# Optimization experiments

Measured on AMD Instinct MI355X. Metric: run time of the kernel, lower is better.

Reference implementation:

```python
import jax, jax.numpy as jnp
import numpy as np

K = 20
EPS = 1e-5
NEG_SLOPE = 0.2


def setup_inputs() -> dict:
    key = jax.random.key(0)
    k1, k2, k3, k4 = jax.random.split(key, 4)
    B, C, N, O = 8, 64, 4096, 64
    x = jax.random.normal(k1, (B, C, N), dtype=jnp.float32)
    # Conv2d(2C, O, kernel_size=1, bias=False) -> weight [O, 2C]
    W = jax.random.normal(k2, (O, 2 * C), dtype=jnp.float32) * (1.0 / np.sqrt(2 * C))
    gamma = jnp.ones((O,), dtype=jnp.float32)
    beta = jnp.zeros((O,), dtype=jnp.float32)
    return {"x": x, "W": W, "gamma": gamma, "beta": beta}


def reference(x, W, gamma, beta):
    B, C, N = x.shape
    xt = jnp.transpose(x, (0, 2, 1))  # [B, N, C]
    # knn: negative squared pairwise distance, topk -> nearest neighbors
    inner = jnp.einsum('bic,bjc->bij', xt, xt)  # [B, N, N]
    xx = jnp.sum(xt * xt, axis=-1)              # [B, N]
    neg_dist = 2.0 * inner - xx[:, :, None] - xx[:, None, :]
    _, idx = jax.lax.top_k(neg_dist, K)         # [B, N, K]
    # gather neighbor features: [B, N, K, C]
    feature = jax.vmap(lambda f, i: f[i])(xt, idx)
    x_central = jnp.broadcast_to(xt[:, :, None, :], (B, N, K, C))
    edge = jnp.concatenate([feature - x_central, x_central], axis=-1)  # [B, N, K, 2C]
    # 1x1 conv == matmul over channel dim
    y = jnp.einsum('bnkc,oc->bnko', edge, W)    # [B, N, K, O]
    # BatchNorm2d in training mode: batch stats over (B, N, K) per channel
    mean = jnp.mean(y, axis=(0, 1, 2))
    var = jnp.var(y, axis=(0, 1, 2))
    y = (y - mean) * jax.lax.rsqrt(var + EPS) * gamma + beta
    y = jnp.where(y >= 0, y, NEG_SLOPE * y)     # LeakyReLU(0.2)
    out = jnp.max(y, axis=2)                    # max over k neighbors -> [B, N, O]
    return jnp.transpose(out, (0, 2, 1))        # [B, O, N]
```

## Files before the change

kernel.cpp:

```cpp
#include <hip/hip_runtime.h>
#include <cstdint>
#include <cstddef>

#define BB 8
#define CC 64
#define NN 4096
#define OO 64
#define KK 20
#define TWO_C 128
#define BN (BB * NN)

#define GSPLIT 16
#define GJPB (NN / GSPLIT)
#define CSPLIT 4
#define CJPB (NN / CSPLIT)
#define SEGCAP 32

typedef float vf4 __attribute__((ext_vector_type(4)));
typedef float f4  __attribute__((ext_vector_type(4)));
typedef _Float16 hf2 __attribute__((ext_vector_type(2)));
typedef _Float16 h8  __attribute__((ext_vector_type(8)));

__device__ __forceinline__ unsigned int pack_h2(float a, float b) {
    hf2 h; h.x = (_Float16)a; h.y = (_Float16)b;
    return __builtin_bit_cast(unsigned int, h);
}

__device__ __forceinline__ unsigned int fmap(float d) {
    unsigned int s = __float_as_uint(d);
    return s ^ (unsigned int)(((int)s >> 31) | 0x80000000);
}

__device__ __forceinline__ unsigned long long cmpx(unsigned long long key, int lane, int j, bool dirDesc) {
    unsigned long long o = __shfl_xor(key, j, 64);
    bool lower = (lane & j) == 0;
    bool takeMax = (dirDesc == lower);
    return ((o > key) == takeMax) ? o : key;
}

__global__ __launch_bounds__(256) void transpose_kernel(const float* __restrict__ x,
                                                        float* __restrict__ xT,
                                                        unsigned int* __restrict__ xTh) {
    __shared__ float t[64][65];
    const int b = blockIdx.y;
    const int n0 = blockIdx.x * 64;
    const int tid = threadIdx.x;
    const int ln = tid & 63, g = tid >> 6;
#pragma unroll
    for (int i = 0; i < 16; ++i) {
        int c = g * 16 + i;
        t[c][ln] = x[((size_t)b * CC + c) * NN + n0 + ln];
    }
    __syncthreads();
#pragma unroll
    for (int i = 0; i < 16; ++i) {
        int nl = g * 16 + i;
        xT[((size_t)b * NN + n0 + nl) * CC + ln] = t[ln][nl];
    }
#pragma unroll
    for (int it = 0; it < 8; ++it) {
        int e = it * 256 + tid;
        int nl = e >> 5, cp = e & 31;
        xTh[((size_t)b * NN + n0 + nl) * 32 + cp] = pack_h2(t[2*cp][nl], t[2*cp+1][nl]);
    }
}

__global__ __launch_bounds__(256) void xx_kernel(const float* __restrict__ x,
                                                 float* __restrict__ xx) {
    int t = blockIdx.x * 256 + threadIdx.x;
    int b = t >> 12, n = t & (NN - 1);
    const float* xp = x + (size_t)b * CC * NN + n;
    float acc = 0.f;
#pragma unroll
    for (int c = 0; c < CC; ++c) {
        float v = xp[(size_t)c * NN];
        acc += v * v;
    }
    xx[t] = acc;
}

__global__ __launch_bounds__(256) void knn_gmax_kernel(const unsigned int* __restrict__ xTh,
                                                       const float* __restrict__ xx,
                                                       float* __restrict__ gmaxG) {
    const int tid = threadIdx.x;
    const int wv = tid >> 6, lane = tid & 63;
    const int lcol = lane & 15, lrow = lane >> 4;
    const int b = blockIdx.z;
    const int i0w = blockIdx.x * 256 + wv * 64;
    const int j0 = blockIdx.y * GJPB;
    const unsigned int* xb = xTh + (size_t)b * NN * 32;
    const float* xxb = xx + (size_t)b * NN;

    uint4 A0[4], A1[4];
#pragma unroll
    for (int s = 0; s < 4; ++s) {
        const uint4* ap = (const uint4*)(xb + (size_t)(i0w + s * 16 + lcol) * 32 + lrow * 4);
        A0[s] = ap[0]; A1[s] = ap[4];
    }

    int g = j0 >> 7;
    for (int gg = 0; gg < GJPB / 128; ++gg, ++g) {
        float m[16];
#pragma unroll
        for (int s = 0; s < 16; ++s) m[s] = -3.4e38f;
#pragma unroll
        for (int jt = 0; jt < 8; ++jt) {
            const int jj = j0 + gg * 128 + jt * 16 + lcol;
            const uint4* bp = (const uint4*)(xb + (size_t)jj * 32 + lrow * 4);
            uint4 B0 = bp[0], B1 = bp[4];
            float h = 0.5f * xxb[jj];
#pragma unroll
            for (int s = 0; s < 4; ++s) {
                f4 acc = {0.f, 0.f, 0.f, 0.f};
                acc = __builtin_amdgcn_mfma_f32_16x16x32_f16(__builtin_bit_cast(h8, A0[s]), __builtin_bit_cast(h8, B0), acc, 0, 0, 0);
                acc = __builtin_amdgcn_mfma_f32_16x16x32_f16(__builtin_bit_cast(h8, A1[s]), __builtin_bit_cast(h8, B1), acc, 0, 0, 0);
#pragma unroll
                for (int r = 0; r < 4; ++r)
                    m[s * 4 + r] = fmaxf(m[s * 4 + r], acc[r] - h);
            }
        }
#pragma unroll
        for (int s = 0; s < 16; ++s) {
#pragma unroll
            for (int off = 1; off < 16; off <<= 1)
                m[s] = fmaxf(m[s], __shfl_xor(m[s], off));
        }
        if (lcol == 0) {
            int r0 = b * NN + i0w + lrow * 4;
#pragma unroll
            for (int s = 0; s < 4; ++s) {
                f4 mv; mv[0] = m[4*s]; mv[1] = m[4*s+1]; mv[2] = m[4*s+2]; mv[3] = m[4*s+3];
                *(f4*)&gmaxG[(size_t)g * BN + r0 + s * 16] = mv;
            }
        }
    }
}

__global__ __launch_bounds__(256) void knn_thresh_kernel(const float* __restrict__ gmaxG,
                                                         float* __restrict__ Tg) {
    const int row = blockIdx.x * 256 + threadIdx.x;
    float L[KK];
#pragma unroll
    for (int s = 0; s < KK; ++s) L[s] = -3.4e38f;
#pragma unroll
    for (int g = 0; g < 32; ++g) {
        float xv = gmaxG[(size_t)g * BN + row];
#pragma unroll
        for (int s = 0; s < KK; ++s) {
            float hi = fmaxf(xv, L[s]);
            xv = fminf(xv, L[s]);
            L[s] = hi;
        }
    }
    Tg[row] = L[KK - 1];
}

__global__ __launch_bounds__(256) void knn_collect_kernel(const unsigned int* __restrict__ xTh,
                                                          const float* __restrict__ xx,
                                                          const float* __restrict__ Tg,
                                                          unsigned short* __restrict__ cand,
                                                          unsigned int* __restrict__ cntS) {
    __shared__ unsigned short bufL[128][SEGCAP];
    __shared__ unsigned int cntL[128];
    const int tid = threadIdx.x;
    const int wv = tid >> 6, lane = tid & 63;
    const int lcol = lane & 15, lrow = lane >> 4;
    const int b = blockIdx.z;
    const int i0 = blockIdx.x * 128;
    const int i0w = i0 + wv * 32;
    const int seg = blockIdx.y;
    const int j0 = seg * CJPB;
    const unsigned int* xb = xTh + (size_t)b * NN * 32;
    const float* xxb = xx + (size_t)b * NN;

    if (tid < 128) cntL[tid] = 0;
    __syncthreads();

    uint4 A0[2], A1[2];
    f4 tt[2];
#pragma unroll
    for (int s = 0; s < 2; ++s) {
        const uint4* ap = (const uint4*)(xb + (size_t)(i0w + s * 16 + lcol) * 32 + lrow * 4);
        A0[s] = ap[0]; A1[s] = ap[4];
        tt[s] = *(const f4*)&Tg[b * NN + i0w + s * 16 + lrow * 4];
    }

#pragma unroll 8
    for (int jt = 0; jt < CJPB / 16; ++jt) {
        const int jj = j0 + jt * 16 + lcol;
        const uint4* bp = (const uint4*)(xb + (size_t)jj * 32 + lrow * 4);
        uint4 B0 = bp[0], B1 = bp[4];
        float h = 0.5f * xxb[jj];
#pragma unroll
        for (int s = 0; s < 2; ++s) {
            f4 acc = {0.f, 0.f, 0.f, 0.f};
            acc = __builtin_amdgcn_mfma_f32_16x16x32_f16(__builtin_bit_cast(h8, A0[s]), __builtin_bit_cast(h8, B0), acc, 0, 0, 0);
            acc = __builtin_amdgcn_mfma_f32_16x16x32_f16(__builtin_bit_cast(h8, A1[s]), __builtin_bit_cast(h8, B1), acc, 0, 0, 0);
#pragma unroll
            for (int r = 0; r < 4; ++r) {
                if (acc[r] - h >= tt[s][r]) {
                    int rl = wv * 32 + s * 16 + lrow * 4 + r;
                    unsigned int slot = atomicAdd(&cntL[rl], 1u);
                    if (slot < SEGCAP) bufL[rl][slot] = (unsigned short)jj;
                }
            }
        }
    }
    __syncthreads();
    const unsigned int* bl = (const unsigned int*)&bufL[0][0];
    unsigned int* cd = (unsigned int*)(cand + ((size_t)seg * BN + b * NN + i0) * SEGCAP);
#pragma unroll
    for (int e = tid; e < 128 * SEGCAP / 2; e += 256) cd[e] = bl[e];
    if (tid < 128) cntS[(size_t)seg * BN + b * NN + i0 + tid] = cntL[tid];
}

__global__ __launch_bounds__(256) void knn_merge_kernel(const float* __restrict__ xT,
                                                        const float* __restrict__ xx,
                                                        const unsigned short* __restrict__ cand,
                                                        const unsigned int* __restrict__ cntS,
                                                        unsigned short* __restrict__ idx_out) {
    const int tid = threadIdx.x;
    const int wv = tid >> 6, lane = tid & 63;
    const int rr = __builtin_amdgcn_readfirstlane(blockIdx.x * 4 + wv);
    const int b = rr >> 12, i = rr & (NN - 1);
    const float* xTb = xT + (size_t)b * NN * CC;
    const float* xxb = xx + b * NN;

    vf4 xiv[CC / 4];
    const float* xip = xTb + (size_t)i * CC;
#pragma unroll
    for (int c4 = 0; c4 < CC / 4; ++c4) xiv[c4] = *(const vf4*)(xip + 4 * c4);

    unsigned int cs[CSPLIT];
    bool segovf = false;
    unsigned int total = 0;
#pragma unroll
    for (int s = 0; s < CSPLIT; ++s) {
        cs[s] = cntS[(size_t)s * BN + rr];
        segovf |= (cs[s] > SEGCAP);
        total += cs[s];
    }

    auto dot_key = [&](int jj) -> unsigned long long {
        const float* xj = xTb + (size_t)jj * CC;
        float a0 = 0.f, a1 = 0.f, a2 = 0.f, a3 = 0.f;
#pragma unroll
        for (int c4 = 0; c4 < CC / 4; ++c4) {
            vf4 xjv = *(const vf4*)(xj + 4 * c4);
            a0 = fmaf(xiv[c4].x, xjv.x, a0);
            a1 = fmaf(xiv[c4].y, xjv.y, a1);
            a2 = fmaf(xiv[c4].z, xjv.z, a2);
            a3 = fmaf(xiv[c4].w, xjv.w, a3);
        }
        float d = 2.f * ((a0 + a1) + (a2 + a3)) - xxb[jj];
        return ((unsigned long long)fmap(d) << 32) | (unsigned int)(NN - 1 - jj);
    };

    auto fetch_key = [&](unsigned int l) -> unsigned long long {
        if (l >= total) return 0ull;
        unsigned int base = 0, addr = 0;
#pragma unroll
        for (int s = 0; s < CSPLIT; ++s) {
            unsigned int lo = base;
            base += cs[s];
            unsigned int a = ((unsigned int)s * (unsigned int)BN + (unsigned int)rr) * SEGCAP + (l - lo);
            bool in = (l >= lo) & (l < base);
            addr = in ? a : addr;
        }
        return dot_key((int)cand[addr]);
    };

    unsigned long long kout;
    if (!segovf && total <= 64) {
        unsigned long long key = fetch_key((unsigned int)lane);
#pragma unroll
        for (int k = 2; k <= 64; k <<= 1) {
            bool dir = (lane & k) == 0;
#pragma unroll
            for (int j = k >> 1; j > 0; j >>= 1) key = cmpx(key, lane, j, dir);
        }
        kout = key;
    } else if (!segovf) {
        unsigned long long key  = fetch_key((unsigned int)lane);
        unsigned long long key2 = fetch_key((unsigned int)lane + 64);
#pragma unroll
        for (int k = 2; k <= 64; k <<= 1) {
            bool dir0 = (lane & k) == 0;
            bool dir1 = (k == 64) ? false : dir0;
#pragma unroll
            for (int j = k >> 1; j > 0; j >>= 1) {
                key  = cmpx(key,  lane, j, dir0);
                key2 = cmpx(key2, lane, j, dir1);
            }
        }
        {
            unsigned long long mx = key2 > key ? key2 : key;
            unsigned long long mn = key2 > key ? key : key2;
            key = mx; key2 = mn;
        }
#pragma unroll
        for (int j = 32; j > 0; j >>= 1) {
            key  = cmpx(key,  lane, j, true);
            key2 = cmpx(key2, lane, j, true);
        }
        kout = key;
    } else {
        unsigned long long run = 0ull;
        for (int t = 0; t < NN / 64; ++t) {
            unsigned long long key = dot_key(t * 64 + lane);
#pragma unroll
            for (int k = 2; k <= 64; k <<= 1) {
                bool dir = (lane & k) == 0;
#pragma unroll
                for (int j = k >> 1; j > 0; j >>= 1) key = cmpx(key, lane, j, dir);
            }
            unsigned long long rev = __shfl(run, 63 - lane, 64);
            key = key > rev ? key : rev;
#pragma unroll
            for (int j = 32; j > 0; j >>= 1) key = cmpx(key, lane, j, true);
            run = key;
        }
        kout = run;
    }

    if (lane < KK)
        idx_out[(size_t)rr * KK + lane] =
            (unsigned short)(NN - 1 - (unsigned int)(kout & 0xFFFFFFFFull));
}

__global__ __launch_bounds__(256) void pd_kernel(const float* __restrict__ x,
                                                 const float* __restrict__ W,
                                                 float* __restrict__ P,
                                                 float* __restrict__ Dd) {
    __shared__ float w1T[CC][32];
    __shared__ float wdT[CC][32];
    const int tid = threadIdx.x;
    const int b = blockIdx.y;
    const int o0 = blockIdx.z * 32;
    for (int e = tid; e < 32 * CC; e += 256) {
        int ol = e >> 6, c = e & 63;
        float w1 = W[(o0 + ol) * TWO_C + c];
        float w2 = W[(o0 + ol) * TWO_C + CC + c];
        w1T[c][ol] = w1;
        wdT[c][ol] = w2 - w1;
    }
    __syncthreads();
    const int n = blockIdx.x * 256 + tid;
    float accp[32], accd[32];
#pragma unroll
    for (int i = 0; i < 32; ++i) { accp[i] = 0.f; accd[i] = 0.f; }
    const float* xp = x + (size_t)b * CC * NN + n;
    for (int c = 0; c < CC; ++c) {
        float xv = xp[(size_t)c * NN];
        const float4* w1r = (const float4*)&w1T[c][0];
        const float4* wdr = (const float4*)&wdT[c][0];
#pragma unroll
        for (int g = 0; g < 8; ++g) {
            float4 aw = w1r[g]; float4 bw = wdr[g];
            accp[4*g+0] += xv * aw.x; accp[4*g+1] += xv * aw.y;
            accp[4*g+2] += xv * aw.z; accp[4*g+3] += xv * aw.w;
            accd[4*g+0] += xv * bw.x; accd[4*g+1] += xv * bw.y;
            accd[4*g+2] += xv * bw.z; accd[4*g+3] += xv * bw.w;
        }
    }
    size_t base = ((size_t)b * NN + n) * OO + o0;
#pragma unroll
    for (int g = 0; g < 8; ++g) {
        *(float4*)&P[base + 4*g]  = make_float4(accp[4*g], accp[4*g+1], accp[4*g+2], accp[4*g+3]);
        *(float4*)&Dd[base + 4*g] = make_float4(accd[4*g], accd[4*g+1], accd[4*g+2], accd[4*g+3]);
    }
}

__global__ __launch_bounds__(256) void stats_kernel(const float* __restrict__ P,
                                                    const float* __restrict__ Dd,
                                                    const unsigned short* __restrict__ idx,
                                                    double* __restrict__ partials) {
    const int tid = threadIdx.x;
    const int o = tid & 63, g = tid >> 6;
    const int row0 = blockIdx.x * 32;
    double s1 = 0.0, s2 = 0.0;
    for (int i = 0; i < 8; ++i) {
        int row = row0 + g + 4 * i;
        int b = row >> 12;
        float d = Dd[(size_t)row * OO + o];
        const unsigned short* ip = idx + (size_t)row * KK;
        const float* Pb = P + ((size_t)b * NN) * OO;
#pragma unroll
        for (int k = 0; k < KK; ++k) {
            int j = ip[k];
            float y = Pb[(size_t)j * OO + o] + d;
            s1 += (double)y;
            s2 += (double)y * (double)y;
        }
    }
    __shared__ double r1[4][64];
    __shared__ double r2[4][64];
    r1[g][o] = s1; r2[g][o] = s2;
    __syncthreads();
    if (g == 0) {
        double a1 = r1[0][o] + r1[1][o] + r1[2][o] + r1[3][o];
        double a2 = r2[0][o] + r2[1][o] + r2[2][o] + r2[3][o];
        partials[(size_t)blockIdx.x * 128 + o]      = a1;
        partials[(size_t)blockIdx.x * 128 + 64 + o] = a2;
    }
}

#define NSTATB (BB * NN / 32)
__global__ void finalize_kernel(const double* __restrict__ partials,
                                const float* __restrict__ gamma,
                                const float* __restrict__ beta,
                                float* __restrict__ ss) {
    int o = threadIdx.x;
    double s1 = 0.0, s2 = 0.0;
    for (int blk = 0; blk < NSTATB; ++blk) {
        s1 += partials[(size_t)blk * 128 + o];
        s2 += partials[(size_t)blk * 128 + 64 + o];
    }
    const double cnt = (double)BB * NN * KK;
    double mean = s1 / cnt;
    double var = s2 / cnt - mean * mean;
    double rs = 1.0 / sqrt(var + 1e-5);
    double sc = (double)gamma[o] * rs;
    ss[o] = (float)sc;
    ss[64 + o] = (float)((double)beta[o] - mean * sc);
}

__global__ __launch_bounds__(256) void out_kernel(const float* __restrict__ P,
                                                  const float* __restrict__ Dd,
                                                  const unsigned short* __restrict__ idx,
                                                  const float* __restrict__ ss,
                                                  float* __restrict__ out) {
    __shared__ float tile[32][65];
    const int tid = threadIdx.x;
    const int o = tid & 63, g = tid >> 6;
    const int b = blockIdx.y;
    const int n0 = blockIdx.x * 32;
    const float sc = ss[o], sh = ss[64 + o];
    const float* Pb = P + ((size_t)b * NN) * OO;
    for (int i = 0; i < 8; ++i) {
        int nl = g + 4 * i;
        int row = b * NN + n0 + nl;
        float d = Dd[(size_t)row * OO + o];
        const unsigned short* ip = idx + (size_t)row * KK;
        float mv = -__builtin_inff();
#pragma unroll
        for (int k = 0; k < KK; ++k) {
            int j = ip[k];
            float y = Pb[(size_t)j * OO + o] + d;
            float t = y * sc + sh;
            t = (t >= 0.f) ? t : 0.2f * t;
            mv = fmaxf(mv, t);
        }
        tile[nl][o] = mv;
    }
    __syncthreads();
    const int nn = tid & 31, og = tid >> 5;
    for (int i = 0; i < 8; ++i) {
        int oo = og + 8 * i;
        out[((size_t)b * OO + oo) * NN + n0 + nn] = tile[nn][oo];
    }
}

extern "C" void kernel_launch(void* const* d_in, const int* in_sizes, int n_in,
                              void* d_out, int out_size, void* d_ws, size_t ws_size,
                              hipStream_t stream) {
    (void)in_sizes; (void)n_in; (void)out_size; (void)ws_size;
    const float* x     = (const float*)d_in[0];
    const float* W     = (const float*)d_in[1];
    const float* gamma = (const float*)d_in[2];
    const float* beta  = (const float*)d_in[3];
    float* out = (float*)d_out;

    char* ws = (char*)d_ws;
    float*          xx       = (float*)ws;
    float*          xT       = (float*)(ws + 131072);
    unsigned int*   xTh      = (unsigned int*)(ws + 8519680);
    float*          gmaxG    = (float*)(ws + 12713984);
    unsigned short* cand     = (unsigned short*)(ws + 12713984);
    float*          Tg       = (float*)(ws + 21102592);
    unsigned int*   cntS     = (unsigned int*)(ws + 21233664);
    unsigned short* idx      = (unsigned short*)(ws + 8519680);
    float*          P        = (float*)(ws + 131072);
    float*          Dd       = (float*)(ws + 12713984);
    double*         partials = (double*)(ws + 21102592);
    float*          ss       = (float*)(ws + 22151168);

    transpose_kernel<<<dim3(NN / 64, BB), 256, 0, stream>>>(x, xT, xTh);
    xx_kernel<<<dim3(BB * NN / 256), 256, 0, stream>>>(x, xx);
    knn_gmax_kernel<<<dim3(NN / 256, GSPLIT, BB), 256, 0, stream>>>(xTh, xx, gmaxG);
    knn_thresh_kernel<<<dim3(BN / 256), 256, 0, stream>>>(gmaxG, Tg);
    knn_collect_kernel<<<dim3(NN / 128, CSPLIT, BB), 256, 0, stream>>>(xTh, xx, Tg, cand, cntS);
    knn_merge_kernel<<<dim3(BN / 4), 256, 0, stream>>>(xT, xx, cand, cntS, idx);
    pd_kernel<<<dim3(NN / 256, BB, 2), 256, 0, stream>>>(x, W, P, Dd);
    stats_kernel<<<dim3(BN / 32), 256, 0, stream>>>(P, Dd, idx, partials);
    finalize_kernel<<<1, 64, 0, stream>>>(partials, gamma, beta, ss);
    out_kernel<<<dim3(NN / 32, BB), 256, 0, stream>>>(P, Dd, idx, ss, out);
}
```

Before: 349.5 us.

## Stage neighbor tiles in LDS with prefetch, ballot-based candidate append, split pd outputs

The knn collect kernel now loads 128-column chunks of the fp16 feature matrix cooperatively into padded shared memory, prefetching the next chunk into registers while the current one is consumed. This replaces per-wave global loads that were duplicated across the four waves. Per-hit LDS atomics are replaced by wave ballots and popcounts that compute write positions, with counts held in registers. Separately, pd_kernel handles 16 output channels per block instead of 32 and launches twice as many blocks, which lowers register pressure at the cost of re-reading x more often.

```diff
diff --git a/kernel.cpp b/kernel.cpp
--- a/kernel.cpp
+++ b/kernel.cpp
@@ -12,6 +12,7 @@
 
 #define GSPLIT 16
 #define GJPB (NN / GSPLIT)
+#define JCH 128
 #define CSPLIT 4
 #define CJPB (NN / CSPLIT)
 #define SEGCAP 32
@@ -160,8 +161,9 @@
                                                           const float* __restrict__ Tg,
                                                           unsigned short* __restrict__ cand,
                                                           unsigned int* __restrict__ cntS) {
+    __shared__ unsigned int stage[JCH * 36];
+    __shared__ float xxh[JCH];
     __shared__ unsigned short bufL[128][SEGCAP];
-    __shared__ unsigned int cntL[128];
     const int tid = threadIdx.x;
     const int wv = tid >> 6, lane = tid & 63;
     const int lcol = lane & 15, lrow = lane >> 4;
@@ -173,9 +175,6 @@
     const unsigned int* xb = xTh + (size_t)b * NN * 32;
     const float* xxb = xx + (size_t)b * NN;
 
-    if (tid < 128) cntL[tid] = 0;
-    __syncthreads();
-
     uint4 A0[2], A1[2];
     f4 tt[2];
 #pragma unroll
@@ -185,33 +184,72 @@
         tt[s] = *(const f4*)&Tg[b * NN + i0w + s * 16 + lrow * 4];
     }
 
-#pragma unroll 8
-    for (int jt = 0; jt < CJPB / 16; ++jt) {
-        const int jj = j0 + jt * 16 + lcol;
-        const uint4* bp = (const uint4*)(xb + (size_t)jj * 32 + lrow * 4);
-        uint4 B0 = bp[0], B1 = bp[4];
-        float h = 0.5f * xxb[jj];
-#pragma unroll
-        for (int s = 0; s < 2; ++s) {
-            f4 acc = {0.f, 0.f, 0.f, 0.f};
-            acc = __builtin_amdgcn_mfma_f32_16x16x32_f16(__builtin_bit_cast(h8, A0[s]), __builtin_bit_cast(h8, B0), acc, 0, 0, 0);
-            acc = __builtin_amdgcn_mfma_f32_16x16x32_f16(__builtin_bit_cast(h8, A1[s]), __builtin_bit_cast(h8, B1), acc, 0, 0, 0);
-#pragma unroll
-            for (int r = 0; r < 4; ++r) {
-                if (acc[r] - h >= tt[s][r]) {
+    unsigned int cnt[2][4];
+#pragma unroll
+    for (int s = 0; s < 2; ++s)
+#pragma unroll
+        for (int r = 0; r < 4; ++r) cnt[s][r] = 0;
+
+    uint4 pf[4];
+    float pxx;
+    {
+        const uint4* src = (const uint4*)(xb + (size_t)j0 * 32);
+#pragma unroll
+        for (int gi = 0; gi < 4; ++gi) pf[gi] = src[gi * 256 + tid];
+        pxx = xxb[j0 + (tid & 127)];
+    }
+
+    for (int jc = j0; jc < j0 + CJPB; jc += JCH) {
+        __syncthreads();
+#pragma unroll
+        for (int gi = 0; gi < 4; ++gi) {
+            int e4 = gi * 256 + tid;
+            *(uint4*)&stage[(e4 >> 3) * 36 + (e4 & 7) * 4] = pf[gi];
+        }
+        if (tid < JCH) xxh[tid] = 0.5f * pxx;
+        __syncthreads();
+        if (jc + JCH < j0 + CJPB) {
+            const uint4* src = (const uint4*)(xb + (size_t)(jc + JCH) * 32);
+#pragma unroll
+            for (int gi = 0; gi < 4; ++gi) pf[gi] = src[gi * 256 + tid];
+            pxx = xxb[jc + JCH + (tid & 127)];
+        }
+#pragma unroll
+        for (int jt = 0; jt < 8; ++jt) {
+            const uint4* bp = (const uint4*)&stage[(jt * 16 + lcol) * 36 + lrow * 4];
+            uint4 B0 = bp[0], B1 = bp[4];
+            float h = xxh[jt * 16 + lcol];
+            const int jj = jc + jt * 16 + lcol;
+#pragma unroll
+            for (int s = 0; s < 2; ++s) {
+                f4 acc = {0.f, 0.f, 0.f, 0.f};
+                acc = __builtin_amdgcn_mfma_f32_16x16x32_f16(__builtin_bit_cast(h8, A0[s]), __builtin_bit_cast(h8, B0), acc, 0, 0, 0);
+                acc = __builtin_amdgcn_mfma_f32_16x16x32_f16(__builtin_bit_cast(h8, A1[s]), __builtin_bit_cast(h8, B1), acc, 0, 0, 0);
+#pragma unroll
+                for (int r = 0; r < 4; ++r) {
+                    bool hit = (acc[r] - h >= tt[s][r]);
+                    unsigned long long mask = __ballot(hit);
+                    unsigned int grp = (unsigned int)(mask >> (lrow * 16)) & 0xFFFFu;
+                    unsigned int pos = cnt[s][r] + (unsigned int)__popc(grp & ((1u << lcol) - 1u));
                     int rl = wv * 32 + s * 16 + lrow * 4 + r;
-                    unsigned int slot = atomicAdd(&cntL[rl], 1u);
-                    if (slot < SEGCAP) bufL[rl][slot] = (unsigned short)jj;
+                    if (hit && pos < SEGCAP) bufL[rl][pos] = (unsigned short)jj;
+                    cnt[s][r] += (unsigned int)__popc(grp);
                 }
             }
         }
+    }
+    if (lcol == 0) {
+#pragma unroll
+        for (int s = 0; s < 2; ++s)
+#pragma unroll
+            for (int r = 0; r < 4; ++r)
+                cntS[(size_t)seg * BN + b * NN + i0 + wv * 32 + s * 16 + lrow * 4 + r] = cnt[s][r];
     }
     __syncthreads();
     const unsigned int* bl = (const unsigned int*)&bufL[0][0];
     unsigned int* cd = (unsigned int*)(cand + ((size_t)seg * BN + b * NN + i0) * SEGCAP);
 #pragma unroll
     for (int e = tid; e < 128 * SEGCAP / 2; e += 256) cd[e] = bl[e];
-    if (tid < 128) cntS[(size_t)seg * BN + b * NN + i0 + tid] = cntL[tid];
 }
 
 __global__ __launch_bounds__(256) void knn_merge_kernel(const float* __restrict__ xT,
@@ -332,12 +370,12 @@
                                                  const float* __restrict__ W,
                                                  float* __restrict__ P,
                                                  float* __restrict__ Dd) {
-    __shared__ float w1T[CC][32];
-    __shared__ float wdT[CC][32];
+    __shared__ float w1T[CC][16];
+    __shared__ float wdT[CC][16];
     const int tid = threadIdx.x;
     const int b = blockIdx.y;
-    const int o0 = blockIdx.z * 32;
-    for (int e = tid; e < 32 * CC; e += 256) {
+    const int o0 = blockIdx.z * 16;
+    for (int e = tid; e < 16 * CC; e += 256) {
         int ol = e >> 6, c = e & 63;
         float w1 = W[(o0 + ol) * TWO_C + c];
         float w2 = W[(o0 + ol) * TWO_C + CC + c];
@@ -346,16 +384,16 @@
     }
     __syncthreads();
     const int n = blockIdx.x * 256 + tid;
-    float accp[32], accd[32];
-#pragma unroll
-    for (int i = 0; i < 32; ++i) { accp[i] = 0.f; accd[i] = 0.f; }
+    float accp[16], accd[16];
+#pragma unroll
+    for (int i = 0; i < 16; ++i) { accp[i] = 0.f; accd[i] = 0.f; }
     const float* xp = x + (size_t)b * CC * NN + n;
     for (int c = 0; c < CC; ++c) {
         float xv = xp[(size_t)c * NN];
         const float4* w1r = (const float4*)&w1T[c][0];
         const float4* wdr = (const float4*)&wdT[c][0];
 #pragma unroll
-        for (int g = 0; g < 8; ++g) {
+        for (int g = 0; g < 4; ++g) {
             float4 aw = w1r[g]; float4 bw = wdr[g];
             accp[4*g+0] += xv * aw.x; accp[4*g+1] += xv * aw.y;
             accp[4*g+2] += xv * aw.z; accp[4*g+3] += xv * aw.w;
@@ -365,7 +403,7 @@
     }
     size_t base = ((size_t)b * NN + n) * OO + o0;
 #pragma unroll
-    for (int g = 0; g < 8; ++g) {
+    for (int g = 0; g < 4; ++g) {
         *(float4*)&P[base + 4*g]  = make_float4(accp[4*g], accp[4*g+1], accp[4*g+2], accp[4*g+3]);
         *(float4*)&Dd[base + 4*g] = make_float4(accd[4*g], accd[4*g+1], accd[4*g+2], accd[4*g+3]);
     }
@@ -491,7 +529,7 @@
     knn_thresh_kernel<<<dim3(BN / 256), 256, 0, stream>>>(gmaxG, Tg);
     knn_collect_kernel<<<dim3(NN / 128, CSPLIT, BB), 256, 0, stream>>>(xTh, xx, Tg, cand, cntS);
     knn_merge_kernel<<<dim3(BN / 4), 256, 0, stream>>>(xT, xx, cand, cntS, idx);
-    pd_kernel<<<dim3(NN / 256, BB, 2), 256, 0, stream>>>(x, W, P, Dd);
+    pd_kernel<<<dim3(NN / 256, BB, 4), 256, 0, stream>>>(x, W, P, Dd);
     stats_kernel<<<dim3(BN / 32), 256, 0, stream>>>(P, Dd, idx, partials);
     finalize_kernel<<<1, 64, 0, stream>>>(partials, gamma, beta, ss);
     out_kernel<<<dim3(NN / 32, BB), 256, 0, stream>>>(P, Dd, idx, ss, out);
```

After: 332.6 us. 1.05x faster.
